# Kernel tuning notes

Measured on AMD Instinct MI355X. Metric: run time of the kernel, lower is better.

Reference implementation:

```python
import jax, jax.numpy as jnp
import numpy as np

N_NODES = 50000
N_EDGES = 800000
N_FEAT = 128
N_HIDDEN = 64
LRELU_ALPHA = 0.05


def setup_inputs() -> dict:
    key = jax.random.key(0)
    k1, k2, k3, k4, k5 = jax.random.split(key, 5)
    x = jax.random.normal(k1, (N_NODES, N_FEAT), dtype=jnp.float32)
    edge_index = jax.random.randint(k2, (2, N_EDGES), 0, N_NODES, dtype=jnp.int64)
    # params (scaled like typical inits to keep exp() in range)
    W_fc = jax.random.normal(k3, (N_FEAT, N_HIDDEN), dtype=jnp.float32) / np.sqrt(N_FEAT)
    a_w = jax.random.normal(k4, (2 * N_HIDDEN, 1), dtype=jnp.float32) / np.sqrt(2 * N_HIDDEN)
    a_b = jax.random.normal(k5, (1,), dtype=jnp.float32) * 0.01
    return {"x": x, "edge_index": edge_index, "W_fc": W_fc, "a_w": a_w, "a_b": a_b}


def reference(x, edge_index, W_fc, a_w, a_b):
    # z = fc(x)                                  [N, H]
    z = x @ W_fc
    dst = edge_index[0]  # row indices (segment ids for softmax)
    src = edge_index[1]  # col indices
    # cat([z[dst], z[src]]) @ a_w + a_b  ==  z[dst]@a1 + z[src]@a2 + b
    nh = z.shape[1]
    s_dst = (z @ a_w[:nh]).squeeze(-1)   # [N] per-node partial scores
    s_src = (z @ a_w[nh:]).squeeze(-1)   # [N]
    h = s_dst[dst] + s_src[src] + a_b[0]          # [E]
    h = jnp.where(h >= 0, h, LRELU_ALPHA * h)     # LeakyReLU
    h = jnp.exp(h)                                # [E]
    # segment softmax over destination node
    h_sum = jax.ops.segment_sum(h, dst, num_segments=x.shape[0])  # [N]
    alpha = h / h_sum[dst]                        # [E]
    # sparse mm: out[i] = sum_{(i,j) in E} alpha_ij * z[j]
    out = jax.ops.segment_sum(alpha[:, None] * z[src], dst, num_segments=x.shape[0])
    return out, alpha
```

## Files before the change

### kernel.cpp

```cpp
#include <hip/hip_runtime.h>
#include <hip/hip_bf16.h>

#define NN 50000
#define NE 800000
#define NF 128
#define NH 64
#define LRELU 0.05f
#define NTILES (NN / 16)
#define SLOT 64
#define BKT 32
#define NB ((NN + BKT - 1) / BKT)
#define CAP 704
#define KB 64
#define EPB (NE / KB)

typedef __attribute__((ext_vector_type(8))) short bf16x8;
typedef __attribute__((ext_vector_type(4))) float f32x4;
typedef __attribute__((ext_vector_type(4))) unsigned int u32x4;

static __device__ inline short f2bf(float f) {
    __hip_bfloat16 h = __float2bfloat16(f);
    return *reinterpret_cast<short*>(&h);
}

__global__ __launch_bounds__(128) void k0_build_bt(
    const float* __restrict__ W, const float* __restrict__ a_w,
    __hip_bfloat16* __restrict__ Bt, int* __restrict__ cursor)
{
    const int c = blockIdx.x, k = threadIdx.x;
    const int gid = c * 128 + k;
    if (gid < NB) cursor[gid] = 0;

    float v = 0.f;
    if (c < NH) {
        v = W[k * NH + c];
    } else if (c == NH) {
        #pragma unroll 8
        for (int h = 0; h < NH; ++h) v = fmaf(W[k * NH + h], a_w[h], v);
    } else if (c == NH + 1) {
        #pragma unroll 8
        for (int h = 0; h < NH; ++h) v = fmaf(W[k * NH + h], a_w[NH + h], v);
    }
    Bt[c * NF + k] = __float2bfloat16(v);
}

__global__ __launch_bounds__(256) void k1_gemm(
    const float* __restrict__ x, const __hip_bfloat16* __restrict__ Bt,
    __hip_bfloat16* __restrict__ z16,
    float* __restrict__ s_dst, float* __restrict__ s_src)
{
    const int wave = threadIdx.x >> 6, lane = threadIdx.x & 63;
    const int tile = blockIdx.x * 4 + wave;
    if (tile >= NTILES) return;
    const int r0   = tile * 16;
    const int lrow = lane & 15;
    const int lgrp = lane >> 4;

    bf16x8 bfrag[5][4];
    #pragma unroll
    for (int n = 0; n < 5; ++n)
        #pragma unroll
        for (int t = 0; t < 4; ++t)
            bfrag[n][t] = *(const bf16x8*)&Bt[(n * 16 + lrow) * NF + t * 32 + lgrp * 8];

    bf16x8 afrag[4];
    const float* xrow = x + (size_t)(r0 + lrow) * NF + lgrp * 8;
    #pragma unroll
    for (int t = 0; t < 4; ++t) {
        f32x4 u = *(const f32x4*)(xrow + t * 32);
        f32x4 v = *(const f32x4*)(xrow + t * 32 + 4);
        bf16x8 a;
        #pragma unroll
        for (int j = 0; j < 4; ++j) { a[j] = f2bf(u[j]); a[4 + j] = f2bf(v[j]); }
        afrag[t] = a;
    }

    f32x4 acc[5] = {};
    #pragma unroll
    for (int t = 0; t < 4; ++t)
        #pragma unroll
        for (int n = 0; n < 5; ++n)
            acc[n] = __builtin_amdgcn_mfma_f32_16x16x32_bf16(afrag[t], bfrag[n][t], acc[n], 0, 0, 0);

    #pragma unroll
    for (int n = 0; n < 4; ++n)
        #pragma unroll
        for (int r = 0; r < 4; ++r)
            z16[(size_t)(r0 + lgrp * 4 + r) * NH + n * 16 + lrow] = __float2bfloat16(acc[n][r]);

    #pragma unroll
    for (int r = 0; r < 4; ++r) {
        const int orow = r0 + lgrp * 4 + r;
        if (lrow == 0)      s_dst[orow] = acc[4][r];
        else if (lrow == 1) s_src[orow] = acc[4][r];
    }
}

__global__ __launch_bounds__(1024) void kC_partition(
    const int* __restrict__ ei, int* __restrict__ cursor,
    unsigned* __restrict__ recs)
{
    __shared__ unsigned hist[NB];
    __shared__ unsigned basel[NB];
    const int tid = threadIdx.x;
    for (int i = tid; i < NB; i += 1024) hist[i] = 0;
    __syncthreads();

    const int base = blockIdx.x * EPB;
    for (int i = tid; i < EPB; i += 1024)
        atomicAdd(&hist[ei[base + i] >> 5], 1u);
    __syncthreads();

    for (int b = tid; b < NB; b += 1024) {
        const unsigned c = hist[b];
        basel[b] = c ? (unsigned)atomicAdd(&cursor[b], (int)c) : 0u;
        hist[b] = 0;
    }
    __syncthreads();

    for (int i = tid; i < EPB; i += 1024) {
        const int d = ei[base + i];
        const int s = ei[NE + base + i];
        const int b = d >> 5;
        const unsigned r = basel[b] + atomicAdd(&hist[b], 1u);
        if (r < CAP)
            recs[(size_t)b * CAP + r] = (unsigned)s | ((unsigned)(d & 31) << 16);
    }
}

__global__ __launch_bounds__(512) void kD_aggregate(
    const __hip_bfloat16* __restrict__ z16,
    const float* __restrict__ s_dst, const float* __restrict__ s_src,
    const float* __restrict__ a_b,
    const unsigned* __restrict__ recs, const int* __restrict__ cursor,
    float* __restrict__ rinv_arr, float* __restrict__ out)
{
    __shared__ unsigned bins[BKT * SLOT];
    __shared__ unsigned lcnt[BKT];
    __shared__ float    sdl[BKT];
    const int bkt = blockIdx.x;
    const int tid = threadIdx.x;
    const int n0  = bkt * BKT;

    if (tid < BKT) {
        lcnt[tid] = 0;
        sdl[tid] = (n0 + tid < NN) ? s_dst[n0 + tid] : 0.f;
    }
    __syncthreads();

    int tot = cursor[bkt];
    if (tot > CAP) tot = CAP;
    const float bias = a_b[0];

    for (int i = tid; i < tot; i += 512) {
        const unsigned rec = recs[(size_t)bkt * CAP + i];
        const unsigned src = rec & 0xffffu;
        const unsigned dl  = (rec >> 16) & 31u;
        float h = sdl[dl] + s_src[src] + bias;
        h = (h >= 0.f) ? h : LRELU * h;
        h = expf(h);
        const unsigned r = atomicAdd(&lcnt[dl], 1u);
        if (r < SLOT)
            bins[dl * SLOT + r] = src | ((unsigned)(unsigned short)f2bf(h) << 16);
    }
    __syncthreads();

    const int wave = tid >> 6, lane = tid & 63;
    const int sub  = lane >> 3, col8 = lane & 7;
    const char* zb = (const char*)z16;

    for (int dl = wave; dl < BKT; dl += 8) {
        const int node = n0 + dl;
        if (node >= NN) break;
        int deg = (int)__builtin_amdgcn_readfirstlane(lcnt[dl]);
        if (deg > SLOT) deg = SLOT;

        unsigned pv = (lane < deg) ? bins[dl * SLOT + lane] : 0u;
        float hs = __uint_as_float(pv & 0xffff0000u);
        float acc[8] = {0.f, 0.f, 0.f, 0.f, 0.f, 0.f, 0.f, 0.f};

        const int gmax = (deg + 7) >> 3;
        for (int g = 0; g < gmax; ++g) {
            const unsigned pg = (unsigned)__builtin_amdgcn_ds_bpermute(
                ((g << 3) | sub) << 2, (int)pv);
            const float hg = __uint_as_float(pg & 0xffff0000u);
            const unsigned sg = pg & 0xffffu;
            const u32x4 q = *(const u32x4*)(zb + ((size_t)(sg << 7) | (col8 << 4)));
            #pragma unroll
            for (int i = 0; i < 4; ++i) {
                acc[2*i]   = fmaf(hg, __uint_as_float(q[i] << 16),         acc[2*i]);
                acc[2*i+1] = fmaf(hg, __uint_as_float(q[i] & 0xffff0000u), acc[2*i+1]);
            }
        }

        #pragma unroll
        for (int off = 8; off <= 32; off <<= 1)
            #pragma unroll
            for (int i = 0; i < 8; ++i) acc[i] += __shfl_xor(acc[i], off, 64);

        #pragma unroll
        for (int off = 32; off > 0; off >>= 1) hs += __shfl_xor(hs, off, 64);
        const float rinv = (deg > 0) ? 1.f / hs : 0.f;
        if (lane == 0) rinv_arr[node] = rinv;

        if (lane < 8) {
            f32x4 o0 = {acc[0] * rinv, acc[1] * rinv, acc[2] * rinv, acc[3] * rinv};
            f32x4 o1 = {acc[4] * rinv, acc[5] * rinv, acc[6] * rinv, acc[7] * rinv};
            float* op = out + (size_t)node * NH + lane * 8;
            *(f32x4*)op       = o0;
            *(f32x4*)(op + 4) = o1;
        }
    }
}

__global__ __launch_bounds__(256) void k7_alpha(
    const int* __restrict__ ei,
    const float* __restrict__ s_dst, const float* __restrict__ s_src,
    const float* __restrict__ a_b, const float* __restrict__ rinv_arr,
    float* __restrict__ alpha)
{
    const int e = blockIdx.x * 256 + threadIdx.x;
    if (e >= NE) return;
    const int d = ei[e];
    const int s = ei[NE + e];
    float h = s_dst[d] + s_src[s] + a_b[0];
    h = (h >= 0.f) ? h : LRELU * h;
    alpha[e] = expf(h) * rinv_arr[d];
}

extern "C" void kernel_launch(void* const* d_in, const int* in_sizes, int n_in,
                              void* d_out, int out_size, void* d_ws, size_t ws_size,
                              hipStream_t stream) {
    const float* x   = (const float*)d_in[0];
    const int*   ei  = (const int*)d_in[1];
    const float* W   = (const float*)d_in[2];
    const float* a_w = (const float*)d_in[3];
    const float* a_b = (const float*)d_in[4];

    float* out   = (float*)d_out;
    float* alpha = out + (size_t)NN * NH;

    __hip_bfloat16* z16 = (__hip_bfloat16*)d_ws;
    __hip_bfloat16* Bt  = z16 + (size_t)NN * NH;
    float* s_dst  = (float*)(Bt + 80 * NF);
    float* s_src  = s_dst + NN;
    float* rinv   = s_src + NN;
    int* cursor   = (int*)(rinv + NN);
    unsigned* recs = (unsigned*)(cursor + NB);

    k0_build_bt <<<80, 128, 0, stream>>>(W, a_w, Bt, cursor);
    k1_gemm     <<<(NTILES + 3) / 4, 256, 0, stream>>>(x, Bt, z16, s_dst, s_src);
    kC_partition<<<KB, 1024, 0, stream>>>(ei, cursor, recs);
    kD_aggregate<<<NB, 512, 0, stream>>>(z16, s_dst, s_src, a_b, recs, cursor, rinv, out);
    k7_alpha    <<<(NE + 255) / 256, 256, 0, stream>>>(ei, s_dst, s_src, a_b, rinv, alpha);
}
```

Measured before the change: 83.56 us.

## Partition edges with more blocks and single-pass register-held ranks

The edge partition kernel now runs on 256 blocks instead of 64, so each block handles 3125 edges and every thread holds at most four edges in registers. The histogram atomic now also returns each edge's local rank, which is kept with the packed record, so the second read of edge_index and the second round of shared atomics go away. This raises parallelism on the GPU and halves edge-index traffic, but it quadruples global cursor atomics, and the unrolled four-slot scheme only covers all edges when EPB is at most 4096.

```diff
diff --git a/kernel.cpp b/kernel.cpp
--- a/kernel.cpp
+++ b/kernel.cpp
@@ -11,7 +11,7 @@
 #define BKT 32
 #define NB ((NN + BKT - 1) / BKT)
 #define CAP 704
-#define KB 64
+#define KB 256
 #define EPB (NE / KB)
 
 typedef __attribute__((ext_vector_type(8))) short bf16x8;
@@ -107,25 +107,42 @@
     __syncthreads();
 
     const int base = blockIdx.x * EPB;
-    for (int i = tid; i < EPB; i += 1024)
-        atomicAdd(&hist[ei[base + i] >> 5], 1u);
+    int      bb0 = -1, bb1 = -1, bb2 = -1, bb3 = -1;
+    unsigned rk0 = 0, rk1 = 0, rk2 = 0, rk3 = 0;
+    unsigned pl0 = 0, pl1 = 0, pl2 = 0, pl3 = 0;
+
+    #define KC_GRAB(J, BBJ, RKJ, PLJ)                                          \
+        { const int i = tid + (J) * 1024;                                      \
+          if (i < EPB) {                                                       \
+              const int d = ei[base + i];                                      \
+              const int s = ei[NE + base + i];                                 \
+              BBJ = d >> 5;                                                    \
+              RKJ = atomicAdd(&hist[BBJ], 1u);                                 \
+              PLJ = (unsigned)s | ((unsigned)(d & 31) << 16);                  \
+          } }
+    KC_GRAB(0, bb0, rk0, pl0)
+    KC_GRAB(1, bb1, rk1, pl1)
+    KC_GRAB(2, bb2, rk2, pl2)
+    KC_GRAB(3, bb3, rk3, pl3)
+    #undef KC_GRAB
     __syncthreads();
 
     for (int b = tid; b < NB; b += 1024) {
         const unsigned c = hist[b];
         basel[b] = c ? (unsigned)atomicAdd(&cursor[b], (int)c) : 0u;
-        hist[b] = 0;
-    }
-    __syncthreads();
-
-    for (int i = tid; i < EPB; i += 1024) {
-        const int d = ei[base + i];
-        const int s = ei[NE + base + i];
-        const int b = d >> 5;
-        const unsigned r = basel[b] + atomicAdd(&hist[b], 1u);
-        if (r < CAP)
-            recs[(size_t)b * CAP + r] = (unsigned)s | ((unsigned)(d & 31) << 16);
-    }
+    }
+    __syncthreads();
+
+    #define KC_PUT(BBJ, RKJ, PLJ)                                              \
+        if (BBJ >= 0) {                                                        \
+            const unsigned pos = basel[BBJ] + RKJ;                             \
+            if (pos < CAP) recs[(size_t)BBJ * CAP + pos] = PLJ;                \
+        }
+    KC_PUT(bb0, rk0, pl0)
+    KC_PUT(bb1, rk1, pl1)
+    KC_PUT(bb2, rk2, pl2)
+    KC_PUT(bb3, rk3, pl3)
+    #undef KC_PUT
 }
 
 __global__ __launch_bounds__(512) void kD_aggregate(
```

New measurement: 79.67 us. 4.7% less time.
